# Optimization experiments

Hardware: AMD Instinct MI355X
Metric: run time of the kernel (lower is better)

The kernel has to match this reference:

```python
import jax, jax.numpy as jnp
import numpy as np

B, S, D, H = 4, 2048, 512, 8
HD = D // H  # head dim = 64
NEG = 1e9


def setup_inputs() -> dict:
    key = jax.random.key(0)
    ks = jax.random.split(key, 10)
    x = jax.random.normal(ks[0], (B, S, D), dtype=jnp.float32)
    group_ids = jnp.sort(jax.random.randint(ks[1], (B, S), 0, 8), axis=-1)
    s = 0.05
    Wq = jax.random.normal(ks[2], (D, D), dtype=jnp.float32) * s
    Wk = jax.random.normal(ks[3], (D, D), dtype=jnp.float32) * s
    Wv = jax.random.normal(ks[4], (D, D), dtype=jnp.float32) * s
    Wo = jax.random.normal(ks[5], (D, D), dtype=jnp.float32) * s
    bq = jnp.zeros((D,), jnp.float32)
    bk = jnp.zeros((D,), jnp.float32)
    bv = jnp.zeros((D,), jnp.float32)
    bo = jnp.zeros((D,), jnp.float32)
    return {"x": x, "group_ids": group_ids, "Wq": Wq, "bq": bq,
            "Wk": Wk, "bk": bk, "Wv": Wv, "bv": bv, "Wo": Wo, "bo": bo}


def reference(x, group_ids, Wq, bq, Wk, bk, Wv, bv, Wo, bo):
    relu = jax.nn.relu
    # projections + activation (activation='relu' is applied to q,k,v AND output)
    q = relu(x @ Wq + bq)  # [B,S,D]
    k = relu(x @ Wk + bk)
    v = relu(x @ Wv + bv)
    # split heads -> [B,H,S,HD]
    def split(t):
        return t.reshape(B, S, H, HD).transpose(0, 2, 1, 3)
    qh, kh, vh = split(q), split(k), split(v)
    # note: scale uses feature dim AFTER head split, i.e. head_dim
    scale = 1.0 / jnp.sqrt(jnp.float32(HD))
    e = jnp.einsum('bhqd,bhkd->bhqk', qh, kh) * scale  # [B,H,S,S]
    group_mask = (group_ids[:, None, :, None] == group_ids[:, None, None, :])  # [B,1,S,S]
    e = e - (1.0 - group_mask.astype(jnp.float32)) * NEG
    a = jax.nn.softmax(e, axis=-1)
    yh = jnp.einsum('bhqk,bhkd->bhqd', a, vh)  # [B,H,S,HD]
    y = yh.transpose(0, 2, 1, 3).reshape(B, S, D)
    return relu(y @ Wo + bo)
```

## Files before the change

kernel.cpp:

```cpp
#include <hip/hip_runtime.h>
#include <cmath>

#define Bsz 4
#define Ssz 2048
#define Dsz 512
#define Hn 8

typedef unsigned short u16;
typedef _Float16 f16;
typedef __attribute__((ext_vector_type(4))) _Float16 f16x4;
typedef __attribute__((ext_vector_type(8))) _Float16 f16x8;
typedef __attribute__((ext_vector_type(8))) unsigned short us8;
typedef __attribute__((ext_vector_type(4))) float f32x4;

__device__ __forceinline__ void gl2lds16(const void* g, void* l) {
    __builtin_amdgcn_global_load_lds(
        (const __attribute__((address_space(1))) void*)g,
        (__attribute__((address_space(3))) void*)l, 16, 0, 0);
}

__global__ __launch_bounds__(256) void conv_x(const float* __restrict__ x,
                                              f16* __restrict__ xb) {
    int i = blockIdx.x * 256 + threadIdx.x;
    const float4* xv = (const float4*)x;
    float4 a = xv[2 * i], b = xv[2 * i + 1];
    f16x8 o;
    o[0] = (f16)a.x; o[1] = (f16)a.y; o[2] = (f16)a.z; o[3] = (f16)a.w;
    o[4] = (f16)b.x; o[5] = (f16)b.y; o[6] = (f16)b.z; o[7] = (f16)b.w;
    ((f16x8*)xb)[i] = o;
}

__global__ __launch_bounds__(256) void conv_w(const float* __restrict__ Wq,
                                              const float* __restrict__ Wk,
                                              const float* __restrict__ Wv,
                                              const float* __restrict__ Wo,
                                              f16* __restrict__ Wtqkv,
                                              f16* __restrict__ Wto) {
    __shared__ float T[64][65];
    const int z = blockIdx.z;
    const float* W = (z == 0) ? Wq : (z == 1) ? Wk : (z == 2) ? Wv : Wo;
    const int n0 = blockIdx.x * 64, k0 = blockIdx.y * 64;
    const int tid = threadIdx.x;
#pragma unroll
    for (int i = 0; i < 16; i++) {
        int e = tid + i * 256;
        int r = e >> 6, c = e & 63;
        T[r][c] = W[(size_t)(k0 + r) * Dsz + n0 + c];
    }
    __syncthreads();
    f16* dst = (z < 3) ? (Wtqkv + ((size_t)z * 512 + n0) * Dsz + k0)
                       : (Wto + (size_t)n0 * Dsz + k0);
#pragma unroll
    for (int i = 0; i < 16; i++) {
        int e = tid + i * 256;
        int r = e >> 6, c = e & 63;
        dst[(size_t)r * Dsz + c] = (f16)(T[c][r]);
    }
}

template <int MODE>
__global__ __launch_bounds__(256) void gemm128(
    const f16* __restrict__ A, const f16* __restrict__ Bt,
    f16* o0, f16* o1, u16* o2v,
    const float* b0, const float* b1, const float* b2,
    float* ofp, const float* bias_f) {
    __shared__ __align__(16) u16 smem[2 * 128 * 64];
    u16* As = smem;
    u16* Bs = smem + 128 * 64;
    const int tid = threadIdx.x;
    const int colg0 = blockIdx.x * 128;
    const int row0 = blockIdx.y * 128;
    const int w = tid >> 6, lane = tid & 63;
    const int ln = lane & 15, quad = lane >> 4;
    const int wr = w >> 1, wc = w & 1;

    f32x4 acc[4][4];
    const f32x4 z4 = {0.f, 0.f, 0.f, 0.f};
#pragma unroll
    for (int bi = 0; bi < 4; bi++)
#pragma unroll
        for (int bj = 0; bj < 4; bj++) acc[bi][bj] = z4;

    const f16* Ablk = A + (size_t)row0 * 512;
    const f16* Bblk = Bt + (size_t)colg0 * 512;

    for (int k0 = 0; k0 < 512; k0 += 64) {
        __syncthreads();
#pragma unroll
        for (int i = 0; i < 4; i++) {
            int p = tid + i * 256;
            int m = p >> 3, kc = p & 7;
            int gk = ((kc ^ (m & 7)) << 3);
            gl2lds16(Ablk + (size_t)m * 512 + k0 + gk, As + p * 8);
            gl2lds16(Bblk + (size_t)m * 512 + k0 + gk, Bs + p * 8);
        }
        __syncthreads();
#pragma unroll
        for (int kk2 = 0; kk2 < 2; kk2++) {
            f16x8 af[4], bfr[4];
#pragma unroll
            for (int bi = 0; bi < 4; bi++) {
                int r = wr * 64 + bi * 16 + ln;
                int ch = r * 8 + ((kk2 * 4 + quad) ^ (r & 7));
                af[bi] = *(const f16x8*)(As + ch * 8);
            }
#pragma unroll
            for (int bj = 0; bj < 4; bj++) {
                int n = wc * 64 + bj * 16 + ln;
                int ch = n * 8 + ((kk2 * 4 + quad) ^ (n & 7));
                bfr[bj] = *(const f16x8*)(Bs + ch * 8);
            }
#pragma unroll
            for (int bi = 0; bi < 4; bi++)
#pragma unroll
                for (int bj = 0; bj < 4; bj++)
                    acc[bi][bj] = __builtin_amdgcn_mfma_f32_16x16x32_f16(
                        af[bi], bfr[bj], acc[bi][bj], 0, 0, 0);
        }
    }

    if (MODE == 0) {
        const int sel = colg0 >> 9;
        const int c0 = colg0 & 511;
        if (sel < 2) {
            f16* outp = (sel == 0) ? o0 : o1;
            const float* bp = (sel == 0) ? b0 : b1;
#pragma unroll
            for (int bj = 0; bj < 4; bj++) {
                int col = c0 + wc * 64 + bj * 16 + ln;
                float bv = bp[col];
#pragma unroll
                for (int bi = 0; bi < 4; bi++)
#pragma unroll
                    for (int r = 0; r < 4; r++) {
                        int row = row0 + wr * 64 + bi * 16 + quad * 4 + r;
                        outp[(size_t)row * 512 + col] =
                            (f16)fmaxf(acc[bi][bj][r] + bv, 0.f);
                    }
            }
        } else {
            const int hh = c0 >> 6;
            f16 (*T)[136] = (f16(*)[136])smem;
            const int bb = row0 >> 11;
            const int t0 = (row0 & 2047) >> 6;
            __syncthreads();
#pragma unroll
            for (int ph = 0; ph < 2; ph++) {
                if (wc == ph) {
#pragma unroll
                    for (int bj = 0; bj < 4; bj++) {
                        int d = bj * 16 + ln;
                        float bv = b2[c0 + ph * 64 + d];
#pragma unroll
                        for (int bi = 0; bi < 4; bi++)
#pragma unroll
                            for (int r = 0; r < 4; r++) {
                                int s = wr * 64 + bi * 16 + quad * 4 + r;
                                T[d][s] = (f16)fmaxf(acc[bi][bj][r] + bv, 0.f);
                            }
                    }
                }
                __syncthreads();
#pragma unroll
                for (int ii = 0; ii < 4; ii++) {
                    int oct = tid + ii * 256;
                    int tt = oct >> 9, rem = oct & 511;
                    int d = rem >> 3, s8 = rem & 7;
                    us8 val = *(const us8*)(&T[d][tt * 64 + s8 * 8]);
                    size_t dst = (((size_t)((bb * 8 + hh + ph) * 32 + t0 + tt)) << 12)
                                 + d * 64 + s8 * 8;
                    *(us8*)(o2v + dst) = val;
                }
                __syncthreads();
            }
        }
    } else {
#pragma unroll
        for (int bj = 0; bj < 4; bj++) {
            int col = colg0 + wc * 64 + bj * 16 + ln;
            float bv = bias_f[col];
#pragma unroll
            for (int bi = 0; bi < 4; bi++)
#pragma unroll
                for (int r = 0; r < 4; r++) {
                    int row = row0 + wr * 64 + bi * 16 + quad * 4 + r;
                    ofp[(size_t)row * 512 + col] = fmaxf(acc[bi][bj][r] + bv, 0.f);
                }
        }
    }
}

__global__ __launch_bounds__(256) void attn_mfma(
    const f16* __restrict__ Q, const f16* __restrict__ K,
    const u16* __restrict__ VT, const int* __restrict__ G,
    f16* __restrict__ Y) {
    __shared__ __align__(16) u16 Ks[2][4096];
    __shared__ __align__(16) u16 Vs[2][4096];

    const int qt = blockIdx.x, h = blockIdx.y, b = blockIdx.z;
    const int q0 = qt * 64;
    const int tid = threadIdx.x;
    const int w = tid >> 6, lane = tid & 63;
    const int ln = lane & 15, quad = lane >> 4;

    const f16* Qb = Q + (size_t)b * Ssz * Dsz;
    const f16* Kb = K + (size_t)b * Ssz * Dsz;
    const u16* Vtb = VT + (size_t)(b * Hn + h) * 32 * 4096;
    const int* Gb = G + (size_t)b * Ssz;

    f16x4 qf[4];
    {
        const f16* qrow = Qb + (size_t)(q0 + w * 16 + ln) * Dsz + h * 64 + quad * 4;
#pragma unroll
        for (int ds = 0; ds < 4; ds++) qf[ds] = *(const f16x4*)(qrow + ds * 16);
    }
    const int gq = Gb[q0 + w * 16 + ln];
    const int gqmin = Gb[q0], gqmax = Gb[q0 + 63];

    int gf = 0, gl = 0; bool ov = false;
    if (lane < 32) {
        gf = Gb[lane * 64]; gl = Gb[lane * 64 + 63];
        ov = (gl >= gqmin) && (gf <= gqmax);
    }
    unsigned long long mask = __ballot(ov);
    const int kt_lo = __builtin_ctzll(mask);
    const int kt_hi = 63 - __builtin_clzll(mask);

    f32x4 o[4];
    const f32x4 z4 = {0.f, 0.f, 0.f, 0.f};
#pragma unroll
    for (int nd = 0; nd < 4; nd++) o[nd] = z4;
    float lsum = 0.f;

#define STAGE_K(kt, bi_)                                                       \
    {                                                                          \
        const f16* Ktile = Kb + (size_t)(kt) * 64 * Dsz + h * 64;              \
        _Pragma("unroll") for (int i = 0; i < 2; i++) {                        \
            int p = tid + i * 256;                                             \
            int row = p >> 3, c = p & 7;                                       \
            gl2lds16(Ktile + (size_t)row * Dsz + ((c ^ (row & 7)) << 3),       \
                     Ks[bi_] + p * 8);                                         \
        }                                                                      \
    }
#define STAGE_V(kt, bi_)                                                       \
    {                                                                          \
        const u16* Vtile = Vtb + (size_t)(kt) * 4096;                          \
        _Pragma("unroll") for (int i = 0; i < 2; i++) {                        \
            int p = tid + i * 256;                                             \
            int row = p >> 3, c = p & 7;                                       \
            gl2lds16(Vtile + row * 64 + ((c ^ (row & 7)) << 3),                \
                     Vs[bi_] + p * 8);                                         \
        }                                                                      \
    }

    STAGE_K(kt_lo, 0)
    STAGE_V(kt_lo, 0)

    int buf = 0;
    for (int kt = kt_lo; kt <= kt_hi; kt++) {
        __syncthreads();
        if (kt < kt_hi) { STAGE_K(kt + 1, buf ^ 1) STAGE_V(kt + 1, buf ^ 1) }
        const u16* ks = Ks[buf];
        const u16* vs = Vs[buf];
        const int k0 = kt * 64;
        const int gkf = __shfl(gf, kt), gkl = __shfl(gl, kt);
        const bool needMask = !(gqmin == gqmax && gkf == gkl);

        f16x4 pf[4];
#pragma unroll
        for (int kb = 0; kb < 4; kb++) {
            f32x4 s = z4;
#pragma unroll
            for (int ds = 0; ds < 4; ds++) {
                int addr = (((kb * 16 + ln) * 8 +
                             ((ds * 2 + (quad >> 1)) ^ (ln & 7))) << 3) +
                           (quad & 1) * 4;
                f16x4 kf = *(const f16x4*)(ks + addr);
                s = __builtin_amdgcn_mfma_f32_16x16x16f16(kf, qf[ds], s, 0, 0, 0);
            }
            float sv[4];
            if (needMask) {
                int4 g4 = *(const int4*)(Gb + k0 + kb * 16 + quad * 4);
                sv[0] = (gq == g4.x) ? s[0] * 0.125f - 4.0f : -1e9f;
                sv[1] = (gq == g4.y) ? s[1] * 0.125f - 4.0f : -1e9f;
                sv[2] = (gq == g4.z) ? s[2] * 0.125f - 4.0f : -1e9f;
                sv[3] = (gq == g4.w) ? s[3] * 0.125f - 4.0f : -1e9f;
            } else {
#pragma unroll
                for (int r = 0; r < 4; r++) sv[r] = s[r] * 0.125f - 4.0f;
            }
            f16x4 pp;
#pragma unroll
            for (int r = 0; r < 4; r++) {
                float e = __expf(sv[r]);
                lsum += e;
                pp[r] = (f16)e;
            }
            pf[kb] = pp;
        }
#pragma unroll
        for (int nd = 0; nd < 4; nd++)
#pragma unroll
            for (int kc = 0; kc < 4; kc++) {
                int addr = (((nd * 16 + ln) * 8 +
                             ((kc * 2 + (quad >> 1)) ^ (ln & 7))) << 3) +
                           (quad & 1) * 4;
                f16x4 vf = *(const f16x4*)(vs + addr);
                o[nd] = __builtin_amdgcn_mfma_f32_16x16x16f16(pf[kc], vf, o[nd], 0, 0, 0);
            }
        buf ^= 1;
    }

    lsum += __shfl_xor(lsum, 16);
    lsum += __shfl_xor(lsum, 32);
    float linv = 1.0f / lsum;
#pragma unroll
    for (int r = 0; r < 4; r++) {
        float lr = __shfl(linv, (lane & 48) | (quad * 4 + r));
        size_t row = (size_t)b * Ssz + q0 + w * 16 + quad * 4 + r;
#pragma unroll
        for (int nd = 0; nd < 4; nd++)
            Y[row * Dsz + h * 64 + nd * 16 + ln] = (f16)(o[nd][r] * lr);
    }
#undef STAGE_K
#undef STAGE_V
}

extern "C" void kernel_launch(void* const* d_in, const int* in_sizes, int n_in,
                              void* d_out, int out_size, void* d_ws, size_t ws_size,
                              hipStream_t stream) {
    const float* x  = (const float*)d_in[0];
    const int*   g  = (const int*)d_in[1];
    const float* Wq = (const float*)d_in[2];
    const float* bq = (const float*)d_in[3];
    const float* Wk = (const float*)d_in[4];
    const float* bk = (const float*)d_in[5];
    const float* Wv = (const float*)d_in[6];
    const float* bv = (const float*)d_in[7];
    const float* Wo = (const float*)d_in[8];
    const float* bo = (const float*)d_in[9];
    float* out = (float*)d_out;

    const size_t E = (size_t)Bsz * Ssz * Dsz;
    f16* xb  = (f16*)d_ws;
    f16* qb  = xb + E;
    f16* kb2 = qb + E;
    u16* vtb = (u16*)(kb2 + E);
    f16* yb  = (f16*)(vtb + E);
    f16* Wtqkv = yb + E;
    f16* Wto   = Wtqkv + 1536 * 512;

    conv_x<<<2048, 256, 0, stream>>>(x, xb);
    conv_w<<<dim3(8, 8, 4), 256, 0, stream>>>(Wq, Wk, Wv, Wo, Wtqkv, Wto);
    gemm128<0><<<dim3(12, 64), 256, 0, stream>>>(xb, Wtqkv, qb, kb2, vtb,
                                                 bq, bk, bv, nullptr, nullptr);
    attn_mfma<<<dim3(Ssz / 64, Hn, Bsz), 256, 0, stream>>>(qb, kb2, vtb, g, yb);
    gemm128<1><<<dim3(4, 64), 256, 0, stream>>>(yb, Wto, nullptr, nullptr, nullptr,
                                                nullptr, nullptr, nullptr, out, bo);
}
```

Baseline: 159.8 us.

## Merge conversion kernels and widen attention blocks to 128 queries

Folds the x and weight conversion kernels into one launch, which removes one kernel launch. Doubles the attention block to 512 threads covering 128 query rows, so every staged K/V tile is reused by eight waves instead of four and each thread now issues a single async load per tile. The trade-offs are half as many attention blocks, a wider group-overlap key range per block (more masked tiles), and higher per-block resource use. The hidden code (output write, masking, loop body) has to stay consistent with the 128-row tiling.

```diff
diff --git a/kernel.cpp b/kernel.cpp
--- a/kernel.cpp
+++ b/kernel.cpp
@@ -19,28 +19,31 @@
         (__attribute__((address_space(3))) void*)l, 16, 0, 0);
 }
 
-__global__ __launch_bounds__(256) void conv_x(const float* __restrict__ x,
-                                              f16* __restrict__ xb) {
-    int i = blockIdx.x * 256 + threadIdx.x;
-    const float4* xv = (const float4*)x;
-    float4 a = xv[2 * i], b = xv[2 * i + 1];
-    f16x8 o;
-    o[0] = (f16)a.x; o[1] = (f16)a.y; o[2] = (f16)a.z; o[3] = (f16)a.w;
-    o[4] = (f16)b.x; o[5] = (f16)b.y; o[6] = (f16)b.z; o[7] = (f16)b.w;
-    ((f16x8*)xb)[i] = o;
-}
-
-__global__ __launch_bounds__(256) void conv_w(const float* __restrict__ Wq,
-                                              const float* __restrict__ Wk,
-                                              const float* __restrict__ Wv,
-                                              const float* __restrict__ Wo,
-                                              f16* __restrict__ Wtqkv,
-                                              f16* __restrict__ Wto) {
+__global__ __launch_bounds__(256) void prep(const float* __restrict__ x,
+                                            f16* __restrict__ xb,
+                                            const float* __restrict__ Wq,
+                                            const float* __restrict__ Wk,
+                                            const float* __restrict__ Wv,
+                                            const float* __restrict__ Wo,
+                                            f16* __restrict__ Wtqkv,
+                                            f16* __restrict__ Wto) {
+    const int blk = blockIdx.x;
+    const int tid = threadIdx.x;
+    if (blk < 2048) {
+        int i = blk * 256 + tid;
+        const float4* xv = (const float4*)x;
+        float4 a = xv[2 * i], b = xv[2 * i + 1];
+        f16x8 o;
+        o[0] = (f16)a.x; o[1] = (f16)a.y; o[2] = (f16)a.z; o[3] = (f16)a.w;
+        o[4] = (f16)b.x; o[5] = (f16)b.y; o[6] = (f16)b.z; o[7] = (f16)b.w;
+        ((f16x8*)xb)[i] = o;
+        return;
+    }
     __shared__ float T[64][65];
-    const int z = blockIdx.z;
+    const int bz = blk - 2048;
+    const int z = bz >> 6;
+    const int n0 = (bz & 7) * 64, k0 = ((bz >> 3) & 7) * 64;
     const float* W = (z == 0) ? Wq : (z == 1) ? Wk : (z == 2) ? Wv : Wo;
-    const int n0 = blockIdx.x * 64, k0 = blockIdx.y * 64;
-    const int tid = threadIdx.x;
 #pragma unroll
     for (int i = 0; i < 16; i++) {
         int e = tid + i * 256;
@@ -190,7 +193,7 @@
     }
 }
 
-__global__ __launch_bounds__(256) void attn_mfma(
+__global__ __launch_bounds__(512) void attn_mfma(
     const f16* __restrict__ Q, const f16* __restrict__ K,
     const u16* __restrict__ VT, const int* __restrict__ G,
     f16* __restrict__ Y) {
@@ -198,7 +201,7 @@
     __shared__ __align__(16) u16 Vs[2][4096];
 
     const int qt = blockIdx.x, h = blockIdx.y, b = blockIdx.z;
-    const int q0 = qt * 64;
+    const int q0 = qt * 128;
     const int tid = threadIdx.x;
     const int w = tid >> 6, lane = tid & 63;
     const int ln = lane & 15, quad = lane >> 4;
@@ -215,7 +218,7 @@
         for (int ds = 0; ds < 4; ds++) qf[ds] = *(const f16x4*)(qrow + ds * 16);
     }
     const int gq = Gb[q0 + w * 16 + ln];
-    const int gqmin = Gb[q0], gqmax = Gb[q0 + 63];
+    const int gqmin = Gb[q0], gqmax = Gb[q0 + 127];
 
     int gf = 0, gl = 0; bool ov = false;
     if (lane < 32) {
@@ -235,22 +238,16 @@
 #define STAGE_K(kt, bi_)                                                       \
     {                                                                          \
         const f16* Ktile = Kb + (size_t)(kt) * 64 * Dsz + h * 64;              \
-        _Pragma("unroll") for (int i = 0; i < 2; i++) {                        \
-            int p = tid + i * 256;                                             \
-            int row = p >> 3, c = p & 7;                                       \
-            gl2lds16(Ktile + (size_t)row * Dsz + ((c ^ (row & 7)) << 3),       \
-                     Ks[bi_] + p * 8);                                         \
-        }                                                                      \
+        int row = tid >> 3, c = tid & 7;                                       \
+        gl2lds16(Ktile + (size_t)row * Dsz + ((c ^ (row & 7)) << 3),           \
+                 Ks[bi_] + tid * 8);                                           \
     }
 #define STAGE_V(kt, bi_)                                                       \
     {                                                                          \
         const u16* Vtile = Vtb + (size_t)(kt) * 4096;                          \
-        _Pragma("unroll") for (int i = 0; i < 2; i++) {                        \
-            int p = tid + i * 256;                                             \
-            int row = p >> 3, c = p & 7;                                       \
-            gl2lds16(Vtile + row * 64 + ((c ^ (row & 7)) << 3),                \
-                     Vs[bi_] + p * 8);                                         \
-        }                                                                      \
+        int row = tid >> 3, c = tid & 7;                                       \
+        gl2lds16(Vtile + row * 64 + ((c ^ (row & 7)) << 3),                    \
+                 Vs[bi_] + tid * 8);                                           \
     }
 
     STAGE_K(kt_lo, 0)
@@ -350,11 +347,10 @@
     f16* Wtqkv = yb + E;
     f16* Wto   = Wtqkv + 1536 * 512;
 
-    conv_x<<<2048, 256, 0, stream>>>(x, xb);
-    conv_w<<<dim3(8, 8, 4), 256, 0, stream>>>(Wq, Wk, Wv, Wo, Wtqkv, Wto);
+    prep<<<2304, 256, 0, stream>>>(x, xb, Wq, Wk, Wv, Wo, Wtqkv, Wto);
     gemm128<0><<<dim3(12, 64), 256, 0, stream>>>(xb, Wtqkv, qb, kb2, vtb,
                                                  bq, bk, bv, nullptr, nullptr);
-    attn_mfma<<<dim3(Ssz / 64, Hn, Bsz), 256, 0, stream>>>(qb, kb2, vtb, g, yb);
+    attn_mfma<<<dim3(Ssz / 128, Hn, Bsz), 512, 0, stream>>>(qb, kb2, vtb, g, yb);
     gemm128<1><<<dim3(4, 64), 256, 0, stream>>>(yb, Wto, nullptr, nullptr, nullptr,
                                                 nullptr, nullptr, nullptr, out, bo);
 }
```

New measurement: 155.6 us. 1.03x faster.
